# Optimization experiments

Hardware: AMD Instinct MI355X
Metric: run time of the kernel (lower is better)

## Reference

```python
import jax, jax.numpy as jnp
import numpy as np

N_NODES = 100000
N_EDGES = 3200000
N_GRAPHS = 512
DIM_H = 128
N_LAYERS = 3
N_CLASSES = 10
BN_EPS = 1e-5


def setup_inputs() -> dict:
    key = jax.random.key(0)
    ks = jax.random.split(key, 16)
    s = 1.0 / np.sqrt(DIM_H)
    x = jax.random.normal(ks[0], (N_NODES, DIM_H), dtype=jnp.float32)
    edge_index = jax.random.randint(ks[1], (2, N_EDGES), 0, N_NODES, dtype=jnp.int64)
    batch = jnp.sort(jax.random.randint(ks[2], (N_NODES,), 0, N_GRAPHS, dtype=jnp.int64))
    W1 = jax.random.uniform(ks[3], (N_LAYERS, DIM_H, DIM_H), jnp.float32, -s, s)
    b1 = jax.random.uniform(ks[4], (N_LAYERS, DIM_H), jnp.float32, -s, s)
    gamma = jnp.ones((N_LAYERS, DIM_H), jnp.float32)
    beta = jnp.zeros((N_LAYERS, DIM_H), jnp.float32)
    rmean = 0.1 * jax.random.normal(ks[5], (N_LAYERS, DIM_H), dtype=jnp.float32)
    rvar = jax.random.uniform(ks[6], (N_LAYERS, DIM_H), jnp.float32, 0.5, 1.5)
    W2 = jax.random.uniform(ks[7], (N_LAYERS, DIM_H, DIM_H), jnp.float32, -s, s)
    b2 = jax.random.uniform(ks[8], (N_LAYERS, DIM_H), jnp.float32, -s, s)
    dcat = DIM_H * N_LAYERS
    sf = 1.0 / np.sqrt(dcat)
    Wfin = jax.random.uniform(ks[9], (dcat, dcat), jnp.float32, -sf, sf)
    bfin = jax.random.uniform(ks[10], (dcat,), jnp.float32, -sf, sf)
    Wout = jax.random.uniform(ks[11], (dcat, N_CLASSES), jnp.float32, -sf, sf)
    bout = jax.random.uniform(ks[12], (N_CLASSES,), jnp.float32, -sf, sf)
    return {"x": x, "edge_index": edge_index, "batch": batch, "num_layers": N_LAYERS,
            "W1": W1, "b1": b1, "gamma": gamma, "beta": beta, "rmean": rmean, "rvar": rvar,
            "W2": W2, "b2": b2, "Wfin": Wfin, "bfin": bfin, "Wout": Wout, "bout": bout}


def reference(x, edge_index, batch, num_layers, W1, b1, gamma, beta, rmean, rvar, W2, b2, Wfin, bfin, Wout, bout):
    src, dst = edge_index[0], edge_index[1]
    h = x
    pooled = []
    for i in range(num_layers):
        # GINConv (eps=0): MLP(x + sum_{j in N(i)} x_j)
        aggr = jax.ops.segment_sum(h[src], dst, num_segments=N_NODES)
        z = (h + aggr) @ W1[i] + b1[i]
        # BatchNorm1d in eval mode (running stats)
        z = gamma[i] * (z - rmean[i]) * jax.lax.rsqrt(rvar[i] + BN_EPS) + beta[i]
        z = jax.nn.relu(z)
        h = jax.nn.relu(z @ W2[i] + b2[i])
        # global_add_pool: segment-sum over graph ids
        pooled.append(jax.ops.segment_sum(h, batch, num_segments=N_GRAPHS))
    h_fin = jnp.concatenate(pooled, axis=1)  # [G, dim_h*num_layers]
    h_fin = jax.nn.relu(h_fin @ Wfin + bfin)
    # dropout p=0.5 is identity in eval mode
    logits = h_fin @ Wout + bout
    return logits, jax.nn.log_softmax(logits, axis=1)
```

## Files before the change

### kernel.cpp

```cpp
#include <hip/hip_runtime.h>
#include <stdint.h>

#define N_NODES 100000
#define N_EDGES 3200000
#define N_GRAPHS 512
#define DIM 128
#define M_PAD 100096
#define NGB (M_PAD / 256)
#define NBUCK 391
#define CAP 9216
#define TILE 4096
#define NTILE 782
#define XMM_NB 392

typedef __bf16 bf16x8 __attribute__((ext_vector_type(8)));
typedef float f32x4 __attribute__((ext_vector_type(4)));

__device__ __forceinline__ unsigned short f2bf(float f) {
  unsigned u = __float_as_uint(f);
  u = u + 0x7FFFu + ((u >> 16) & 1u);
  return (unsigned short)(u >> 16);
}
__device__ __forceinline__ float bflo(unsigned v) { return __uint_as_float(v << 16); }
__device__ __forceinline__ float bfhi(unsigned v) { return __uint_as_float(v & 0xFFFF0000u); }
__device__ __forceinline__ float bfs(unsigned short v) { return __uint_as_float(((unsigned)v) << 16); }
__device__ __forceinline__ unsigned packbf(float a, float b) {
  return (unsigned)f2bf(a) | ((unsigned)f2bf(b) << 16);
}

__global__ void k_zero32(int* __restrict__ p, int n) {
  int i = blockIdx.x * 256 + threadIdx.x;
  if (i < n) p[i] = 0;
}

__global__ __launch_bounds__(256) void k_bucket(const int* __restrict__ ei,
                                                int* __restrict__ cnt,
                                                unsigned* __restrict__ rec) {
  __shared__ int hist[NBUCK];
  __shared__ int curs[NBUCK];
  int t = threadIdx.x;
  int base_e = blockIdx.x * TILE;
  int es[16], ed[16];
#pragma unroll
  for (int k = 0; k < 16; ++k) {
    int e = base_e + k * 256 + t;
    if (e < N_EDGES) { es[k] = ei[e]; ed[k] = ei[N_EDGES + e]; }
    else ed[k] = -1;
  }
  for (int i = t; i < NBUCK; i += 256) hist[i] = 0;
  __syncthreads();
#pragma unroll
  for (int k = 0; k < 16; ++k)
    if (ed[k] >= 0) atomicAdd(&hist[ed[k] >> 8], 1);
  __syncthreads();
  for (int i = t; i < NBUCK; i += 256) {
    int h = hist[i];
    int g = h ? atomicAdd(&cnt[i], h) : 0;
    curs[i] = i * CAP + g;
  }
  __syncthreads();
#pragma unroll
  for (int k = 0; k < 16; ++k) {
    if (ed[k] >= 0) {
      int b = ed[k] >> 8;
      int pos = atomicAdd(&curs[b], 1);
      rec[pos] = ((unsigned)es[k] << 8) | (unsigned)(ed[k] & 255);
    }
  }
}

__global__ __launch_bounds__(512) void k_bscan(const int* __restrict__ cnt,
                                               int* __restrict__ bbase,
                                               int* __restrict__ row_ptr) {
  __shared__ int sc[512];
  int t = threadIdx.x;
  int tot = (t < NBUCK) ? min(cnt[t], CAP) : 0;
  sc[t] = tot; __syncthreads();
  for (int off = 1; off < 512; off <<= 1) {
    int x = (t >= off) ? sc[t - off] : 0;
    __syncthreads();
    sc[t] += x;
    __syncthreads();
  }
  if (t < NBUCK) bbase[t] = sc[t] - tot;
  if (t == NBUCK - 1) {
    bbase[NBUCK] = sc[t];
    row_ptr[N_NODES] = sc[t];
  }
}

__global__ __launch_bounds__(256) void k_build(const unsigned* __restrict__ rec,
                                               const int* __restrict__ cnt,
                                               const int* __restrict__ bbase,
                                               int* __restrict__ row_ptr,
                                               int* __restrict__ col) {
  __shared__ int hist[256];
  __shared__ int sc[256];
  __shared__ int curs[256];
  int b = blockIdx.x, t = threadIdx.x;
  int n = min(cnt[b], CAP);
  const unsigned* p = rec + (size_t)b * CAP;
  hist[t] = 0; __syncthreads();
  for (int i = t; i < n; i += 256) atomicAdd(&hist[p[i] & 255u], 1);
  __syncthreads();
  int v = hist[t];
  sc[t] = v; __syncthreads();
  for (int off = 1; off < 256; off <<= 1) {
    int x = (t >= off) ? sc[t - off] : 0;
    __syncthreads();
    sc[t] += x;
    __syncthreads();
  }
  int excl = bbase[b] + sc[t] - v;
  int node = (b << 8) + t;
  if (node < N_NODES) row_ptr[node] = excl;
  curs[t] = excl;
  __syncthreads();
  for (int i = t; i < n; i += 256) {
    unsigned w = p[i];
    int pos = atomicAdd(&curs[w & 255u], 1);
    col[pos] = (int)(w >> 8);
  }
}

__global__ __launch_bounds__(256) void k_xmm1(const float* __restrict__ x,
                                              float* __restrict__ pmax,
                                              float* __restrict__ pmin) {
  __shared__ float smx[8][32][4];
  __shared__ float smn[8][32][4];
  int t = threadIdx.x;
  int c4 = t & 31;
  int ro = t >> 5;
  float mx0 = 0.f, mx1 = 0.f, mx2 = 0.f, mx3 = 0.f;
  float mn0 = 0.f, mn1 = 0.f, mn2 = 0.f, mn3 = 0.f;
  for (int row = blockIdx.x * 8 + ro; row < N_NODES; row += XMM_NB * 8) {
    float4 v = ((const float4*)x)[(size_t)row * 32 + c4];
    mx0 = fmaxf(mx0, v.x); mn0 = fmaxf(mn0, -v.x);
    mx1 = fmaxf(mx1, v.y); mn1 = fmaxf(mn1, -v.y);
    mx2 = fmaxf(mx2, v.z); mn2 = fmaxf(mn2, -v.z);
    mx3 = fmaxf(mx3, v.w); mn3 = fmaxf(mn3, -v.w);
  }
  smx[ro][c4][0] = mx0; smx[ro][c4][1] = mx1; smx[ro][c4][2] = mx2; smx[ro][c4][3] = mx3;
  smn[ro][c4][0] = mn0; smn[ro][c4][1] = mn1; smn[ro][c4][2] = mn2; smn[ro][c4][3] = mn3;
  __syncthreads();
  for (int off = 4; off > 0; off >>= 1) {
    if (ro < off) {
#pragma unroll
      for (int k = 0; k < 4; ++k) {
        smx[ro][c4][k] = fmaxf(smx[ro][c4][k], smx[ro + off][c4][k]);
        smn[ro][c4][k] = fmaxf(smn[ro][c4][k], smn[ro + off][c4][k]);
      }
    }
    __syncthreads();
  }
  if (ro == 0) {
#pragma unroll
    for (int k = 0; k < 4; ++k) {
      pmax[blockIdx.x * 128 + c4 * 4 + k] = smx[0][c4][k];
      pmin[blockIdx.x * 128 + c4 * 4 + k] = smn[0][c4][k];
    }
  }
}

__global__ __launch_bounds__(64) void k_xmm2(const float* __restrict__ pmax,
                                             const float* __restrict__ pmin,
                                             float* __restrict__ xmx,
                                             float* __restrict__ xminf) {
  int c = blockIdx.x & 127;
  int isMin = blockIdx.x >> 7;
  const float* src = isMin ? pmin : pmax;
  int l = threadIdx.x;
  float m = 0.f;
  for (int p2 = l; p2 < XMM_NB; p2 += 64) m = fmaxf(m, src[p2 * 128 + c]);
#pragma unroll
  for (int off = 32; off > 0; off >>= 1) m = fmaxf(m, __shfl_down(m, off));
  if (l == 0) {
    if (isMin) xminf[c] = -m;
    else xmx[c] = m;
  }
}

__global__ __launch_bounds__(64) void k_hred(const float* __restrict__ pmaxb,
                                             float* __restrict__ hmax) {
  int c = blockIdx.x;
  float m = 0.f;
  for (int b = threadIdx.x; b < NGB; b += 64) m = fmaxf(m, pmaxb[(size_t)b * 128 + c]);
#pragma unroll
  for (int off = 32; off > 0; off >>= 1) m = fmaxf(m, __shfl_down(m, off));
  if (threadIdx.x == 0) hmax[c] = m;
}

__global__ void k_convx(const float* __restrict__ x, const float* __restrict__ qmin,
                        const float* __restrict__ qmax, unsigned short* __restrict__ xq) {
  int i = blockIdx.x * 256 + threadIdx.x;
  if (i >= M_PAD * 64) return;
  int lane = i & 63;
  unsigned short o = 0;
  if ((i >> 6) < N_NODES) {
    float mn0 = qmin[2 * lane], mn1 = qmin[2 * lane + 1];
    float r0 = qmax[2 * lane] - mn0, r1 = qmax[2 * lane + 1] - mn1;
    float is0 = r0 > 1e-20f ? 255.f / r0 : 0.f;
    float is1 = r1 > 1e-20f ? 255.f / r1 : 0.f;
    float2 f = ((const float2*)x)[i];
    int q0 = (int)rintf((f.x - mn0) * is0); q0 = min(max(q0, 0), 255);
    int q1 = (int)rintf((f.y - mn1) * is1); q1 = min(max(q1, 0), 255);
    o = (unsigned short)(q0 | (q1 << 8));
  }
  xq[i] = o;
}

__global__ void k_quant(const unsigned* __restrict__ hbf, const float* __restrict__ qmax,
                        unsigned short* __restrict__ hq) {
  int i = blockIdx.x * 256 + threadIdx.x;
  if (i >= M_PAD * 64) return;
  int lane = i & 63;
  float mx0 = qmax[2 * lane], mx1 = qmax[2 * lane + 1];
  float is0 = mx0 > 1e-20f ? 255.f / mx0 : 0.f;
  float is1 = mx1 > 1e-20f ? 255.f / mx1 : 0.f;
  unsigned v = hbf[i];
  int q0 = (int)rintf(bflo(v) * is0); q0 = min(max(q0, 0), 255);
  int q1 = (int)rintf(bfhi(v) * is1); q1 = min(max(q1, 0), 255);
  hq[i] = (unsigned short)(q0 | (q1 << 8));
}

__global__ void k_convw(const float* __restrict__ W1, const float* __restrict__ W2,
                        unsigned short* __restrict__ Wt1, unsigned short* __restrict__ Wt2) {
  int i = blockIdx.x * 256 + threadIdx.x;
  if (i >= 3 * DIM * DIM) return;
  int l = i >> 14, rem = i & 16383, k = rem >> 7, n = rem & 127;
  int o = (l << 14) + (n << 7) + k;
  Wt1[o] = f2bf(W1[i]);
  Wt2[o] = f2bf(W2[i]);
}

__global__ void k_coef(const float* __restrict__ b1, const float* __restrict__ gamma,
                       const float* __restrict__ beta, const float* __restrict__ rmean,
                       const float* __restrict__ rvar, const float* __restrict__ b2,
                       float* __restrict__ sA1, float* __restrict__ sB1,
                       float* __restrict__ sA2, float* __restrict__ sB2) {
  int i = blockIdx.x * 128 + threadIdx.x;
  if (i >= 3 * DIM) return;
  float sa = gamma[i] * rsqrtf(rvar[i] + 1e-5f);
  sA1[i] = sa;
  sB1[i] = fmaf(sa, b1[i] - rmean[i], beta[i]);
  sA2[i] = 1.0f;
  sB2[i] = b2[i];
}

__global__ __launch_bounds__(256) void k_aggr(const unsigned short* __restrict__ hq,
                                              const int* __restrict__ row_ptr,
                                              const int* __restrict__ col,
                                              const float* __restrict__ qmin,
                                              const float* __restrict__ qmax,
                                              unsigned* __restrict__ tmp) {
  const unsigned* hq32 = (const unsigned*)hq;
  int wv = (blockIdx.x << 2) + (threadIdx.x >> 6);
  int lane = threadIdx.x & 63;
  int dw = lane & 31;
  bool hi = lane >= 32;
  if (wv >= M_PAD) return;
  if (wv >= N_NODES) {
    ((uint2*)(tmp + (size_t)wv * 64))[dw] = make_uint2(0u, 0u);
    return;
  }
  unsigned ae = 0u, ao = 0u;
  int s = __builtin_amdgcn_readfirstlane(row_ptr[wv]);
  int e = __builtin_amdgcn_readfirstlane(row_ptr[wv + 1]);
  for (int base = s; base < e; base += 64) {
    int n = e - base; if (n > 64) n = 64;
    int cv = (lane < n) ? col[base + lane] : 0;
    int np = n >> 1;
    int j = 0;
    for (; j + 8 <= np; j += 8) {
#pragma unroll
      for (int u = 0; u < 8; ++u) {
        int s0 = __builtin_amdgcn_readlane(cv, 2 * (j + u));
        int s1 = __builtin_amdgcn_readlane(cv, 2 * (j + u) + 1);
        unsigned v = hq32[(hi ? s1 : s0) * 32 + dw];
        ae += v & 0x00FF00FFu;
        ao += (v >> 8) & 0x00FF00FFu;
      }
    }
    for (; j < np; ++j) {
      int s0 = __builtin_amdgcn_readlane(cv, 2 * j);
      int s1 = __builtin_amdgcn_readlane(cv, 2 * j + 1);
      unsigned v = hq32[(hi ? s1 : s0) * 32 + dw];
      ae += v & 0x00FF00FFu;
      ao += (v >> 8) & 0x00FF00FFu;
    }
    if (n & 1) {
      int c = __builtin_amdgcn_readlane(cv, n - 1);
      unsigned v = hq32[c * 32 + dw];
      if (hi) v = 0u;
      ae += v & 0x00FF00FFu;
      ao += (v >> 8) & 0x00FF00FFu;
    }
  }
  ae += __shfl_xor(ae, 32);
  ao += __shfl_xor(ao, 32);
  {
    unsigned v = hq32[wv * 32 + dw];
    ae += v & 0x00FF00FFu;
    ao += (v >> 8) & 0x00FF00FFu;
  }
  if (lane < 32) {
    float cnt = (float)(e - s + 1);
    float4 qn = ((const float4*)qmin)[dw];
    float4 qx = ((const float4*)qmax)[dw];
    const float k255 = 1.0f / 255.0f;
    float A0 = fmaf(qn.x, cnt, (qx.x - qn.x) * k255 * (float)(ae & 0xFFFFu));
    float A1 = fmaf(qn.y, cnt, (qx.y - qn.y) * k255 * (float)(ao & 0xFFFFu));
    float A2 = fmaf(qn.z, cnt, (qx.z - qn.z) * k255 * (float)(ae >> 16));
    float A3 = fmaf(qn.w, cnt, (qx.w - qn.w) * k255 * (float)(ao >> 16));
    ((uint2*)(tmp + (size_t)wv * 64))[dw] = make_uint2(packbf(A0, A1), packbf(A2, A3));
  }
}

__global__ __launch_bounds__(256, 2) void k_gemm12(const unsigned short* __restrict__ A,
                                                   const unsigned short* __restrict__ Wt1,
                                                   const float* __restrict__ sA1,
                                                   const float* __restrict__ sB1,
                                                   const unsigned short* __restrict__ Wt2,
                                                   const float* __restrict__ sA2,
                                                   const float* __restrict__ sB2,
                                                   const int* __restrict__ batch,
                                                   unsigned short* __restrict__ out,
                                                   float* __restrict__ pooled8, int layer,
                                                   float* __restrict__ pmaxb, int do_max) {
  __shared__ unsigned short zt[4][64][136];
  __shared__ float colred[128];
  __shared__ int sgid[256];
  int w = threadIdx.x >> 6, lane = threadIdx.x & 63;
  int q = lane >> 4, n16 = lane & 15;
  int rbase = (blockIdx.x << 8) + (w << 6);
  if (do_max && threadIdx.x < 128) colred[threadIdx.x] = 0.f;
  {
    int rr = (blockIdx.x << 8) + threadIdx.x;
    sgid[threadIdx.x] = (rr < N_NODES) ? batch[rr] : -1;
  }

  {
    bf16x8 Bf[4][8];
#pragma unroll
    for (int ks = 0; ks < 4; ++ks)
#pragma unroll
      for (int c = 0; c < 8; ++c)
        Bf[ks][c] = *(const bf16x8*)(Wt1 + (size_t)((c << 4) + n16) * DIM + ks * 32 + q * 8);
#pragma unroll
    for (int t = 0; t < 4; ++t) {
      int r0 = rbase + (t << 4);
      f32x4 acc[8] = {};
#pragma unroll
      for (int ks = 0; ks < 4; ++ks) {
        bf16x8 a = *(const bf16x8*)(A + (size_t)(r0 + n16) * DIM + ks * 32 + q * 8);
#pragma unroll
        for (int c = 0; c < 8; ++c)
          acc[c] = __builtin_amdgcn_mfma_f32_16x16x32_bf16(a, Bf[ks][c], acc[c], 0, 0, 0);
      }
#pragma unroll
      for (int c = 0; c < 8; ++c) {
        int colc = (c << 4) + n16;
        float s = sA1[colc], tt = sB1[colc];
#pragma unroll
        for (int r = 0; r < 4; ++r) {
          float v = fmaxf(fmaf(s, acc[c][r], tt), 0.0f);
          zt[w][(t << 4) + (q << 2) + r][colc] = f2bf(v);
        }
      }
    }
  }

  float mcol[8];
#pragma unroll
  for (int c = 0; c < 8; ++c) mcol[c] = 0.f;
  {
    bf16x8 Bf[4][8];
#pragma unroll
    for (int ks = 0; ks < 4; ++ks)
#pragma unroll
      for (int c = 0; c < 8; ++c)
        Bf[ks][c] = *(const bf16x8*)(Wt2 + (size_t)((c << 4) + n16) * DIM + ks * 32 + q * 8);
#pragma unroll
    for (int t = 0; t < 4; ++t) {
      int r0 = rbase + (t << 4);
      f32x4 acc[8] = {};
#pragma unroll
      for (int ks = 0; ks < 4; ++ks) {
        bf16x8 a = *(const bf16x8*)(&zt[w][(t << 4) + n16][ks * 32 + q * 8]);
#pragma unroll
        for (int c = 0; c < 8; ++c)
          acc[c] = __builtin_amdgcn_mfma_f32_16x16x32_bf16(a, Bf[ks][c], acc[c], 0, 0, 0);
      }
      __builtin_amdgcn_s_waitcnt(0);
#pragma unroll
      for (int c = 0; c < 8; ++c) {
        int colc = (c << 4) + n16;
        float s = sA2[colc], tt = sB2[colc];
#pragma unroll
        for (int r = 0; r < 4; ++r) {
          float v = fmaxf(fmaf(s, acc[c][r], tt), 0.0f);
          mcol[c] = fmaxf(mcol[c], v);
          unsigned short hv = f2bf(v);
          out[(size_t)(r0 + (q << 2) + r) * DIM + colc] = hv;
          zt[w][(t << 4) + (q << 2) + r][colc] = hv;
        }
      }
    }
  }
  __syncthreads();

  {
    const unsigned short* ztf = &zt[0][0][0];
    int colp = threadIdx.x & 127, grp = threadIdx.x >> 7;
    int cp = blockIdx.x & 7;
    float pacc = 0.f;
    int gcur = sgid[grp << 7];
    for (int r = 0; r < 128; ++r) {
      int row = (grp << 7) + r;
      int g = sgid[row];
      if (g != gcur) {
        if (gcur >= 0)
          atomicAdd(&pooled8[((size_t)cp * N_GRAPHS + gcur) * 384 + layer * DIM + colp], pacc);
        pacc = 0.f; gcur = g;
      }
      if (g >= 0) pacc += bfs(ztf[row * 136 + colp]);
    }
    if (gcur >= 0)
      atomicAdd(&pooled8[((size_t)cp * N_GRAPHS + gcur) * 384 + layer * DIM + colp], pacc);
  }

  if (do_max) {
#pragma unroll
    for (int c = 0; c < 8; ++c)
      atomicMax((int*)&colred[(c << 4) + n16], __float_as_int(mcol[c]));
    __syncthreads();
    if (threadIdx.x < 128)
      pmaxb[(size_t)blockIdx.x * 128 + threadIdx.x] = colred[threadIdx.x];
  }
}

__global__ __launch_bounds__(384) void k_head(const float* __restrict__ pooled8,
                                              const float* __restrict__ Wfin,
                                              const float* __restrict__ bfin,
                                              const float* __restrict__ Wout,
                                              const float* __restrict__ bout,
                                              float* __restrict__ out) {
  __shared__ float p[8][384];
  __shared__ float hf[8][392];
  __shared__ float lg[8][10];
  __shared__ float lse[8];
  int t = threadIdx.x, g0 = blockIdx.x << 3;
  for (int i = t; i < 8 * 384; i += 384) {
    int gl = i / 384, k = i % 384;
    float s = 0.f;
#pragma unroll
    for (int cp = 0; cp < 8; ++cp)
      s += pooled8[((size_t)cp * N_GRAPHS + g0 + gl) * 384 + k];
    p[gl][k] = s;
  }
  __syncthreads();
  float bb = bfin[t];
  float acc[8];
#pragma unroll
  for (int g = 0; g < 8; ++g) acc[g] = bb;
  for (int k = 0; k < 384; ++k) {
    float wv = Wfin[k * 384 + t];
#pragma unroll
    for (int g = 0; g < 8; ++g) acc[g] = fmaf(p[g][k], wv, acc[g]);
  }
#pragma unroll
  for (int g = 0; g < 8; ++g) hf[g][t] = fmaxf(acc[g], 0.f);
  __syncthreads();
  if (t < 80) {
    int g = t / 10, c = t % 10;
    float a = bout[c];
    for (int k = 0; k < 384; ++k) a = fmaf(hf[g][k], Wout[k * 10 + c], a);
    lg[g][c] = a;
  }
  __syncthreads();
  if (t < 8) {
    float m = lg[t][0];
#pragma unroll
    for (int i = 1; i < 10; ++i) m = fmaxf(m, lg[t][i]);
    float ss = 0.f;
#pragma unroll
    for (int i = 0; i < 10; ++i) ss += __expf(lg[t][i] - m);
    lse[t] = m + __logf(ss);
  }
  __syncthreads();
  if (t < 80) {
    int g = t / 10, c = t % 10;
    out[(size_t)(g0 + g) * 10 + c] = lg[g][c];
    out[(size_t)N_GRAPHS * 10 + (size_t)(g0 + g) * 10 + c] = lg[g][c] - lse[g];
  }
}

extern "C" void kernel_launch(void* const* d_in, const int* in_sizes, int n_in,
                              void* d_out, int out_size, void* d_ws, size_t ws_size,
                              hipStream_t stream) {
  const float* x     = (const float*)d_in[0];
  const int*   ei    = (const int*)d_in[1];
  const int*   batch = (const int*)d_in[2];
  const float* W1    = (const float*)d_in[4];
  const float* b1    = (const float*)d_in[5];
  const float* gamma = (const float*)d_in[6];
  const float* beta  = (const float*)d_in[7];
  const float* rmean = (const float*)d_in[8];
  const float* rvar  = (const float*)d_in[9];
  const float* W2    = (const float*)d_in[10];
  const float* b2    = (const float*)d_in[11];
  const float* Wfin  = (const float*)d_in[12];
  const float* bfin  = (const float*)d_in[13];
  const float* Wout  = (const float*)d_in[14];
  const float* bout  = (const float*)d_in[15];
  float* out = (float*)d_out;

  char* p = (char*)d_ws;
  auto alloc = [&](size_t bytes) { char* r = p; p += (bytes + 255) & ~255ull; return r; };
  int* cnt      = (int*)alloc(NBUCK * 4);
  unsigned* rec = (unsigned*)alloc((size_t)NBUCK * CAP * 4);
  int* bbase    = (int*)alloc((NBUCK + 1) * 4);
  int* row_ptr  = (int*)alloc((N_NODES + 1) * 4);
  int* colb     = (int*)alloc((size_t)N_EDGES * 4);
  unsigned short* xq  = (unsigned short*)alloc((size_t)M_PAD * 64 * 2);
  unsigned short* hqb = (unsigned short*)alloc((size_t)M_PAD * 64 * 2);
  unsigned* hbf  = (unsigned*)alloc((size_t)M_PAD * 64 * 4);
  unsigned* tmpb = (unsigned*)alloc((size_t)M_PAD * 64 * 4);
  unsigned short* Wt1 = (unsigned short*)alloc(3 * DIM * DIM * 2);
  unsigned short* Wt2 = (unsigned short*)alloc(3 * DIM * DIM * 2);
  float* pmax   = (float*)alloc((size_t)XMM_NB * 128 * 4);
  float* pmin   = (float*)alloc((size_t)XMM_NB * 128 * 4);
  float* pmaxb  = (float*)alloc((size_t)NGB * 128 * 4);
  float* sA1    = (float*)alloc(384 * 4);
  float* sB1    = (float*)alloc(384 * 4);
  float* sA2    = (float*)alloc(384 * 4);
  float* sB2    = (float*)alloc(384 * 4);
  float* qbuf   = (float*)alloc(1024 * 4);
  float* xmx    = qbuf + 128;
  float* xminf  = qbuf + 256;
  float* hmax0  = qbuf + 384;
  float* hmax1  = qbuf + 512;
  float* zeros  = qbuf + 640;
  float* pooled8 = (float*)alloc((size_t)8 * N_GRAPHS * 384 * 4);

  k_zero32<<<(NBUCK + 255) / 256, 256, 0, stream>>>(cnt, NBUCK);
  k_zero32<<<4, 256, 0, stream>>>((int*)qbuf, 1024);
  k_zero32<<<(8 * N_GRAPHS * 384 + 255) / 256, 256, 0, stream>>>((int*)pooled8, 8 * N_GRAPHS * 384);

  k_bucket<<<NTILE, 256, 0, stream>>>(ei, cnt, rec);
  k_bscan<<<1, 512, 0, stream>>>(cnt, bbase, row_ptr);
  k_build<<<NBUCK, 256, 0, stream>>>(rec, cnt, bbase, row_ptr, colb);

  k_xmm1<<<XMM_NB, 256, 0, stream>>>(x, pmax, pmin);
  k_xmm2<<<256, 64, 0, stream>>>(pmax, pmin, xmx, xminf);
  k_convx<<<(M_PAD * 64 + 255) / 256, 256, 0, stream>>>(x, xminf, xmx, xq);
  k_convw<<<(3 * DIM * DIM + 255) / 256, 256, 0, stream>>>(W1, W2, Wt1, Wt2);
  k_coef<<<3, 128, 0, stream>>>(b1, gamma, beta, rmean, rvar, b2, sA1, sB1, sA2, sB2);

  k_aggr<<<M_PAD / 4, 256, 0, stream>>>(xq, row_ptr, colb, xminf, xmx, tmpb);
  k_gemm12<<<NGB, 256, 0, stream>>>((const unsigned short*)tmpb, Wt1, sA1, sB1,
                                    Wt2, sA2, sB2, batch, (unsigned short*)hbf,
                                    pooled8, 0, pmaxb, 1);
  k_hred<<<128, 64, 0, stream>>>(pmaxb, hmax0);
  k_quant<<<(M_PAD * 64 + 255) / 256, 256, 0, stream>>>(hbf, hmax0, hqb);
  k_aggr<<<M_PAD / 4, 256, 0, stream>>>(hqb, row_ptr, colb, zeros, hmax0, tmpb);
  k_gemm12<<<NGB, 256, 0, stream>>>((const unsigned short*)tmpb, Wt1 + DIM * DIM,
                                    sA1 + DIM, sB1 + DIM, Wt2 + DIM * DIM,
                                    sA2 + DIM, sB2 + DIM, batch, (unsigned short*)hbf,
                                    pooled8, 1, pmaxb, 1);
  k_hred<<<128, 64, 0, stream>>>(pmaxb, hmax1);
  k_quant<<<(M_PAD * 64 + 255) / 256, 256, 0, stream>>>(hbf, hmax1, hqb);
  k_aggr<<<M_PAD / 4, 256, 0, stream>>>(hqb, row_ptr, colb, zeros, hmax1, tmpb);
  k_gemm12<<<NGB, 256, 0, stream>>>((const unsigned short*)tmpb, Wt1 + 2 * DIM * DIM,
                                    sA1 + 2 * DIM, sB1 + 2 * DIM, Wt2 + 2 * DIM * DIM,
                                    sA2 + 2 * DIM, sB2 + 2 * DIM, batch, (unsigned short*)hbf,
                                    pooled8, 2, pmaxb, 0);

  k_head<<<N_GRAPHS / 8, 384, 0, stream>>>(pooled8, Wfin, bfin, Wout, bout, out);
}
```

Baseline: 659.3 us.

## Gather neighbor rows with 128-bit loads, eight edges per wave step

Rewrites the per-node neighbor aggregation so each wave handles 32 edges per iteration. Lanes split into 8 groups of 8, and each lane loads 16-byte chunks of the quantized rows, replacing the readlane-serialized 4-byte gathers. Out-of-range edges are pointed at a zeroed padding row, which k_quant now clears explicitly. This adds a cross-lane shuffle reduction and a bpermute redistribution at the end in exchange for fewer, wider memory requests.

```diff
diff --git a/kernel.cpp b/kernel.cpp
--- a/kernel.cpp
+++ b/kernel.cpp
@@ -213,6 +213,7 @@
                         unsigned short* __restrict__ hq) {
   int i = blockIdx.x * 256 + threadIdx.x;
   if (i >= M_PAD * 64) return;
+  if ((i >> 6) >= N_NODES) { hq[i] = 0; return; }
   int lane = i & 63;
   float mx0 = qmax[2 * lane], mx1 = qmax[2 * lane + 1];
   float is0 = mx0 > 1e-20f ? 255.f / mx0 : 0.f;
@@ -253,66 +254,93 @@
                                               const float* __restrict__ qmin,
                                               const float* __restrict__ qmax,
                                               unsigned* __restrict__ tmp) {
+  const uint4* hq128 = (const uint4*)hq;
   const unsigned* hq32 = (const unsigned*)hq;
   int wv = (blockIdx.x << 2) + (threadIdx.x >> 6);
   int lane = threadIdx.x & 63;
+  int grp = lane >> 3;
+  int lo8 = lane & 7;
   int dw = lane & 31;
-  bool hi = lane >= 32;
   if (wv >= M_PAD) return;
   if (wv >= N_NODES) {
     ((uint2*)(tmp + (size_t)wv * 64))[dw] = make_uint2(0u, 0u);
     return;
   }
-  unsigned ae = 0u, ao = 0u;
+  unsigned ae0 = 0, ae1 = 0, ae2 = 0, ae3 = 0;
+  unsigned ao0 = 0, ao1 = 0, ao2 = 0, ao3 = 0;
   int s = __builtin_amdgcn_readfirstlane(row_ptr[wv]);
   int e = __builtin_amdgcn_readfirstlane(row_ptr[wv + 1]);
-  for (int base = s; base < e; base += 64) {
-    int n = e - base; if (n > 64) n = 64;
-    int cv = (lane < n) ? col[base + lane] : 0;
-    int np = n >> 1;
-    int j = 0;
-    for (; j + 8 <= np; j += 8) {
-#pragma unroll
-      for (int u = 0; u < 8; ++u) {
-        int s0 = __builtin_amdgcn_readlane(cv, 2 * (j + u));
-        int s1 = __builtin_amdgcn_readlane(cv, 2 * (j + u) + 1);
-        unsigned v = hq32[(hi ? s1 : s0) * 32 + dw];
-        ae += v & 0x00FF00FFu;
-        ao += (v >> 8) & 0x00FF00FFu;
-      }
-    }
-    for (; j < np; ++j) {
-      int s0 = __builtin_amdgcn_readlane(cv, 2 * j);
-      int s1 = __builtin_amdgcn_readlane(cv, 2 * j + 1);
-      unsigned v = hq32[(hi ? s1 : s0) * 32 + dw];
+  int pidx = (lo8 << 3) + grp;
+  for (int base = s; base < e; base += 32) {
+    int n = e - base; if (n > 32) n = 32;
+    int cv = (pidx < n) ? col[base + pidx] : 0;
+    int s0 = __builtin_amdgcn_ds_swizzle(cv, 0x18);
+    int s1 = __builtin_amdgcn_ds_swizzle(cv, 0x38);
+    int s2 = __builtin_amdgcn_ds_swizzle(cv, 0x58);
+    int s3 = __builtin_amdgcn_ds_swizzle(cv, 0x78);
+    s0 = (grp      < n) ? s0 : N_NODES;
+    s1 = (grp +  8 < n) ? s1 : N_NODES;
+    s2 = (grp + 16 < n) ? s2 : N_NODES;
+    s3 = (grp + 24 < n) ? s3 : N_NODES;
+    uint4 v0 = hq128[s0 * 8 + lo8];
+    uint4 v1 = hq128[s1 * 8 + lo8];
+    uint4 v2 = hq128[s2 * 8 + lo8];
+    uint4 v3 = hq128[s3 * 8 + lo8];
+    ae0 += v0.x & 0x00FF00FFu; ao0 += (v0.x >> 8) & 0x00FF00FFu;
+    ae1 += v0.y & 0x00FF00FFu; ao1 += (v0.y >> 8) & 0x00FF00FFu;
+    ae2 += v0.z & 0x00FF00FFu; ao2 += (v0.z >> 8) & 0x00FF00FFu;
+    ae3 += v0.w & 0x00FF00FFu; ao3 += (v0.w >> 8) & 0x00FF00FFu;
+    ae0 += v1.x & 0x00FF00FFu; ao0 += (v1.x >> 8) & 0x00FF00FFu;
+    ae1 += v1.y & 0x00FF00FFu; ao1 += (v1.y >> 8) & 0x00FF00FFu;
+    ae2 += v1.z & 0x00FF00FFu; ao2 += (v1.z >> 8) & 0x00FF00FFu;
+    ae3 += v1.w & 0x00FF00FFu; ao3 += (v1.w >> 8) & 0x00FF00FFu;
+    ae0 += v2.x & 0x00FF00FFu; ao0 += (v2.x >> 8) & 0x00FF00FFu;
+    ae1 += v2.y & 0x00FF00FFu; ao1 += (v2.y >> 8) & 0x00FF00FFu;
+    ae2 += v2.z & 0x00FF00FFu; ao2 += (v2.z >> 8) & 0x00FF00FFu;
+    ae3 += v2.w & 0x00FF00FFu; ao3 += (v2.w >> 8) & 0x00FF00FFu;
+    ae0 += v3.x & 0x00FF00FFu; ao0 += (v3.x >> 8) & 0x00FF00FFu;
+    ae1 += v3.y & 0x00FF00FFu; ao1 += (v3.y >> 8) & 0x00FF00FFu;
+    ae2 += v3.z & 0x00FF00FFu; ao2 += (v3.z >> 8) & 0x00FF00FFu;
+    ae3 += v3.w & 0x00FF00FFu; ao3 += (v3.w >> 8) & 0x00FF00FFu;
+  }
+  ae0 += __shfl_xor(ae0, 8); ae0 += __shfl_xor(ae0, 16); ae0 += __shfl_xor(ae0, 32);
+  ae1 += __shfl_xor(ae1, 8); ae1 += __shfl_xor(ae1, 16); ae1 += __shfl_xor(ae1, 32);
+  ae2 += __shfl_xor(ae2, 8); ae2 += __shfl_xor(ae2, 16); ae2 += __shfl_xor(ae2, 32);
+  ae3 += __shfl_xor(ae3, 8); ae3 += __shfl_xor(ae3, 16); ae3 += __shfl_xor(ae3, 32);
+  ao0 += __shfl_xor(ao0, 8); ao0 += __shfl_xor(ao0, 16); ao0 += __shfl_xor(ao0, 32);
+  ao1 += __shfl_xor(ao1, 8); ao1 += __shfl_xor(ao1, 16); ao1 += __shfl_xor(ao1, 32);
+  ao2 += __shfl_xor(ao2, 8); ao2 += __shfl_xor(ao2, 16); ao2 += __shfl_xor(ao2, 32);
+  ao3 += __shfl_xor(ao3, 8); ao3 += __shfl_xor(ao3, 16); ao3 += __shfl_xor(ao3, 32);
+  {
+    int ba = ((dw >> 2) & 7) << 2;
+    unsigned f0 = (unsigned)__builtin_amdgcn_ds_bpermute(ba, (int)ae0);
+    unsigned f1 = (unsigned)__builtin_amdgcn_ds_bpermute(ba, (int)ae1);
+    unsigned f2 = (unsigned)__builtin_amdgcn_ds_bpermute(ba, (int)ae2);
+    unsigned f3 = (unsigned)__builtin_amdgcn_ds_bpermute(ba, (int)ae3);
+    unsigned g0 = (unsigned)__builtin_amdgcn_ds_bpermute(ba, (int)ao0);
+    unsigned g1 = (unsigned)__builtin_amdgcn_ds_bpermute(ba, (int)ao1);
+    unsigned g2 = (unsigned)__builtin_amdgcn_ds_bpermute(ba, (int)ao2);
+    unsigned g3 = (unsigned)__builtin_amdgcn_ds_bpermute(ba, (int)ao3);
+    unsigned el = (dw & 1) ? f1 : f0;
+    unsigned eh = (dw & 1) ? f3 : f2;
+    unsigned ae = (dw & 2) ? eh : el;
+    unsigned ol = (dw & 1) ? g1 : g0;
+    unsigned oh = (dw & 1) ? g3 : g2;
+    unsigned ao = (dw & 2) ? oh : ol;
+    if (lane < 32) {
+      unsigned v = hq32[wv * 32 + dw];
       ae += v & 0x00FF00FFu;
       ao += (v >> 8) & 0x00FF00FFu;
+      float cntf = (float)(e - s + 1);
+      float4 qn = ((const float4*)qmin)[dw];
+      float4 qx = ((const float4*)qmax)[dw];
+      const float k255 = 1.0f / 255.0f;
+      float A0 = fmaf(qn.x, cntf, (qx.x - qn.x) * k255 * (float)(ae & 0xFFFFu));
+      float A1 = fmaf(qn.y, cntf, (qx.y - qn.y) * k255 * (float)(ao & 0xFFFFu));
+      float A2 = fmaf(qn.z, cntf, (qx.z - qn.z) * k255 * (float)(ae >> 16));
+      float A3 = fmaf(qn.w, cntf, (qx.w - qn.w) * k255 * (float)(ao >> 16));
+      ((uint2*)(tmp + (size_t)wv * 64))[dw] = make_uint2(packbf(A0, A1), packbf(A2, A3));
     }
-    if (n & 1) {
-      int c = __builtin_amdgcn_readlane(cv, n - 1);
-      unsigned v = hq32[c * 32 + dw];
-      if (hi) v = 0u;
-      ae += v & 0x00FF00FFu;
-      ao += (v >> 8) & 0x00FF00FFu;
-    }
-  }
-  ae += __shfl_xor(ae, 32);
-  ao += __shfl_xor(ao, 32);
-  {
-    unsigned v = hq32[wv * 32 + dw];
-    ae += v & 0x00FF00FFu;
-    ao += (v >> 8) & 0x00FF00FFu;
-  }
-  if (lane < 32) {
-    float cnt = (float)(e - s + 1);
-    float4 qn = ((const float4*)qmin)[dw];
-    float4 qx = ((const float4*)qmax)[dw];
-    const float k255 = 1.0f / 255.0f;
-    float A0 = fmaf(qn.x, cnt, (qx.x - qn.x) * k255 * (float)(ae & 0xFFFFu));
-    float A1 = fmaf(qn.y, cnt, (qx.y - qn.y) * k255 * (float)(ao & 0xFFFFu));
-    float A2 = fmaf(qn.z, cnt, (qx.z - qn.z) * k255 * (float)(ae >> 16));
-    float A3 = fmaf(qn.w, cnt, (qx.w - qn.w) * k255 * (float)(ao >> 16));
-    ((uint2*)(tmp + (size_t)wv * 64))[dw] = make_uint2(packbf(A0, A1), packbf(A2, A3));
   }
 }
 
```

After: 621.1 us. 5.8% less time.

## Split quantized features into column teams and aggregate one node per thread

Applied to the files above, without the earlier changes.

The quantized feature matrix is stored as four column slices, each 32 bytes per node, so that each thread can gather a whole node's slice with two 16-byte loads. The aggregation kernel changes from one wavefront per node to one thread per node per team. Each thread loops up to the wavefront's maximum degree, uses a zero padding row for edges past its own degree, and keeps packed 8-bit accumulators in registers. This aims to remove the per-edge readlane and shuffle overhead and issue wider gathers, at the cost of divergence from varying degrees, uncoalesced column-index loads and higher register pressure.

```diff
diff --git a/kernel.cpp b/kernel.cpp
--- a/kernel.cpp
+++ b/kernel.cpp
@@ -12,6 +12,8 @@
 #define TILE 4096
 #define NTILE 782
 #define XMM_NB 392
+#define NTEAM 4
+#define ZROW N_NODES
 
 typedef __bf16 bf16x8 __attribute__((ext_vector_type(8)));
 typedef float f32x4 __attribute__((ext_vector_type(4)));
@@ -195,8 +197,9 @@
   int i = blockIdx.x * 256 + threadIdx.x;
   if (i >= M_PAD * 64) return;
   int lane = i & 63;
+  int node = i >> 6;
   unsigned short o = 0;
-  if ((i >> 6) < N_NODES) {
+  if (node < N_NODES) {
     float mn0 = qmin[2 * lane], mn1 = qmin[2 * lane + 1];
     float r0 = qmax[2 * lane] - mn0, r1 = qmax[2 * lane + 1] - mn1;
     float is0 = r0 > 1e-20f ? 255.f / r0 : 0.f;
@@ -206,7 +209,7 @@
     int q1 = (int)rintf((f.y - mn1) * is1); q1 = min(max(q1, 0), 255);
     o = (unsigned short)(q0 | (q1 << 8));
   }
-  xq[i] = o;
+  xq[(size_t)(lane >> 4) * (M_PAD * 16) + (size_t)node * 16 + (lane & 15)] = o;
 }
 
 __global__ void k_quant(const unsigned* __restrict__ hbf, const float* __restrict__ qmax,
@@ -214,13 +217,16 @@
   int i = blockIdx.x * 256 + threadIdx.x;
   if (i >= M_PAD * 64) return;
   int lane = i & 63;
+  int node = i >> 6;
+  size_t oidx = (size_t)(lane >> 4) * (M_PAD * 16) + (size_t)node * 16 + (lane & 15);
+  if (node >= N_NODES) { hq[oidx] = 0; return; }
   float mx0 = qmax[2 * lane], mx1 = qmax[2 * lane + 1];
   float is0 = mx0 > 1e-20f ? 255.f / mx0 : 0.f;
   float is1 = mx1 > 1e-20f ? 255.f / mx1 : 0.f;
   unsigned v = hbf[i];
   int q0 = (int)rintf(bflo(v) * is0); q0 = min(max(q0, 0), 255);
   int q1 = (int)rintf(bfhi(v) * is1); q1 = min(max(q1, 0), 255);
-  hq[i] = (unsigned short)(q0 | (q1 << 8));
+  hq[oidx] = (unsigned short)(q0 | (q1 << 8));
 }
 
 __global__ void k_convw(const float* __restrict__ W1, const float* __restrict__ W2,
@@ -247,72 +253,80 @@
   sB2[i] = b2[i];
 }
 
+#define ACCP(v, E, O) { E += (v) & 0x00FF00FFu; O += ((v) >> 8) & 0x00FF00FFu; }
+
+__device__ __forceinline__ uint2 dq2(unsigned ev, unsigned od, float4 qn, float4 qx, float cntf) {
+  const float k255 = 1.0f / 255.0f;
+  float A0 = fmaf(qn.x, cntf, (qx.x - qn.x) * k255 * (float)(ev & 0xFFFFu));
+  float A1 = fmaf(qn.y, cntf, (qx.y - qn.y) * k255 * (float)(od & 0xFFFFu));
+  float A2 = fmaf(qn.z, cntf, (qx.z - qn.z) * k255 * (float)(ev >> 16));
+  float A3 = fmaf(qn.w, cntf, (qx.w - qn.w) * k255 * (float)(od >> 16));
+  return make_uint2(packbf(A0, A1), packbf(A2, A3));
+}
+
 __global__ __launch_bounds__(256) void k_aggr(const unsigned short* __restrict__ hq,
                                               const int* __restrict__ row_ptr,
                                               const int* __restrict__ col,
                                               const float* __restrict__ qmin,
                                               const float* __restrict__ qmax,
                                               unsigned* __restrict__ tmp) {
-  const unsigned* hq32 = (const unsigned*)hq;
-  int wv = (blockIdx.x << 2) + (threadIdx.x >> 6);
-  int lane = threadIdx.x & 63;
-  int dw = lane & 31;
-  bool hi = lane >= 32;
-  if (wv >= M_PAD) return;
-  if (wv >= N_NODES) {
-    ((uint2*)(tmp + (size_t)wv * 64))[dw] = make_uint2(0u, 0u);
-    return;
-  }
-  unsigned ae = 0u, ao = 0u;
-  int s = __builtin_amdgcn_readfirstlane(row_ptr[wv]);
-  int e = __builtin_amdgcn_readfirstlane(row_ptr[wv + 1]);
-  for (int base = s; base < e; base += 64) {
-    int n = e - base; if (n > 64) n = 64;
-    int cv = (lane < n) ? col[base + lane] : 0;
-    int np = n >> 1;
-    int j = 0;
-    for (; j + 8 <= np; j += 8) {
-#pragma unroll
-      for (int u = 0; u < 8; ++u) {
-        int s0 = __builtin_amdgcn_readlane(cv, 2 * (j + u));
-        int s1 = __builtin_amdgcn_readlane(cv, 2 * (j + u) + 1);
-        unsigned v = hq32[(hi ? s1 : s0) * 32 + dw];
-        ae += v & 0x00FF00FFu;
-        ao += (v >> 8) & 0x00FF00FFu;
-      }
-    }
-    for (; j < np; ++j) {
-      int s0 = __builtin_amdgcn_readlane(cv, 2 * j);
-      int s1 = __builtin_amdgcn_readlane(cv, 2 * j + 1);
-      unsigned v = hq32[(hi ? s1 : s0) * 32 + dw];
-      ae += v & 0x00FF00FFu;
-      ao += (v >> 8) & 0x00FF00FFu;
-    }
-    if (n & 1) {
-      int c = __builtin_amdgcn_readlane(cv, n - 1);
-      unsigned v = hq32[c * 32 + dw];
-      if (hi) v = 0u;
-      ae += v & 0x00FF00FFu;
-      ao += (v >> 8) & 0x00FF00FFu;
-    }
-  }
-  ae += __shfl_xor(ae, 32);
-  ao += __shfl_xor(ao, 32);
-  {
-    unsigned v = hq32[wv * 32 + dw];
-    ae += v & 0x00FF00FFu;
-    ao += (v >> 8) & 0x00FF00FFu;
-  }
-  if (lane < 32) {
-    float cnt = (float)(e - s + 1);
-    float4 qn = ((const float4*)qmin)[dw];
-    float4 qx = ((const float4*)qmax)[dw];
-    const float k255 = 1.0f / 255.0f;
-    float A0 = fmaf(qn.x, cnt, (qx.x - qn.x) * k255 * (float)(ae & 0xFFFFu));
-    float A1 = fmaf(qn.y, cnt, (qx.y - qn.y) * k255 * (float)(ao & 0xFFFFu));
-    float A2 = fmaf(qn.z, cnt, (qx.z - qn.z) * k255 * (float)(ae >> 16));
-    float A3 = fmaf(qn.w, cnt, (qx.w - qn.w) * k255 * (float)(ao >> 16));
-    ((uint2*)(tmp + (size_t)wv * 64))[dw] = make_uint2(packbf(A0, A1), packbf(A2, A3));
+  int team = blockIdx.x & (NTEAM - 1);
+  int nr = blockIdx.x >> 2;
+  int node = (nr << 8) + threadIdx.x;
+  const uint4* hs = (const uint4*)((const unsigned short*)hq + (size_t)team * (M_PAD * 16));
+  bool valid = node < N_NODES;
+  int s = valid ? row_ptr[node] : 0;
+  int e = valid ? row_ptr[node + 1] : 0;
+  int deg = e - s;
+  int dmax = deg;
+#pragma unroll
+  for (int off = 32; off > 0; off >>= 1) dmax = max(dmax, __shfl_xor(dmax, off));
+
+  unsigned ev[8], od[8];
+#pragma unroll
+  for (int g = 0; g < 8; ++g) { ev[g] = 0u; od[g] = 0u; }
+
+  for (int e0 = 0; e0 < dmax; e0 += 4) {
+    int c[4];
+#pragma unroll
+    for (int u = 0; u < 4; ++u)
+      c[u] = (e0 + u < deg) ? col[s + e0 + u] : ZROW;
+    uint4 ga[4], gb[4];
+#pragma unroll
+    for (int u = 0; u < 4; ++u) {
+      ga[u] = hs[(size_t)c[u] * 2];
+      gb[u] = hs[(size_t)c[u] * 2 + 1];
+    }
+#pragma unroll
+    for (int u = 0; u < 4; ++u) {
+      ACCP(ga[u].x, ev[0], od[0]); ACCP(ga[u].y, ev[1], od[1]);
+      ACCP(ga[u].z, ev[2], od[2]); ACCP(ga[u].w, ev[3], od[3]);
+      ACCP(gb[u].x, ev[4], od[4]); ACCP(gb[u].y, ev[5], od[5]);
+      ACCP(gb[u].z, ev[6], od[6]); ACCP(gb[u].w, ev[7], od[7]);
+    }
+  }
+
+  uint4* dst = (uint4*)(tmp + (size_t)node * 64 + team * 16);
+  if (valid) {
+    uint4 sa = hs[(size_t)node * 2];
+    uint4 sb = hs[(size_t)node * 2 + 1];
+    ACCP(sa.x, ev[0], od[0]); ACCP(sa.y, ev[1], od[1]);
+    ACCP(sa.z, ev[2], od[2]); ACCP(sa.w, ev[3], od[3]);
+    ACCP(sb.x, ev[4], od[4]); ACCP(sb.y, ev[5], od[5]);
+    ACCP(sb.z, ev[6], od[6]); ACCP(sb.w, ev[7], od[7]);
+    float cntf = (float)(deg + 1);
+    const float4* qnp = (const float4*)qmin + team * 8;
+    const float4* qxp = (const float4*)qmax + team * 8;
+    uint2 r[8];
+#pragma unroll
+    for (int g = 0; g < 8; ++g) r[g] = dq2(ev[g], od[g], qnp[g], qxp[g], cntf);
+    dst[0] = make_uint4(r[0].x, r[0].y, r[1].x, r[1].y);
+    dst[1] = make_uint4(r[2].x, r[2].y, r[3].x, r[3].y);
+    dst[2] = make_uint4(r[4].x, r[4].y, r[5].x, r[5].y);
+    dst[3] = make_uint4(r[6].x, r[6].y, r[7].x, r[7].y);
+  } else {
+    uint4 z = make_uint4(0u, 0u, 0u, 0u);
+    dst[0] = z; dst[1] = z; dst[2] = z; dst[3] = z;
   }
 }
 
@@ -521,7 +535,7 @@
   unsigned* rec = (unsigned*)alloc((size_t)NBUCK * CAP * 4);
   int* bbase    = (int*)alloc((NBUCK + 1) * 4);
   int* row_ptr  = (int*)alloc((N_NODES + 1) * 4);
-  int* colb     = (int*)alloc((size_t)N_EDGES * 4);
+  int* colb     = (int*)alloc(((size_t)N_EDGES + 256) * 4);
   unsigned short* xq  = (unsigned short*)alloc((size_t)M_PAD * 64 * 2);
   unsigned short* hqb = (unsigned short*)alloc((size_t)M_PAD * 64 * 2);
   unsigned* hbf  = (unsigned*)alloc((size_t)M_PAD * 64 * 4);
@@ -557,20 +571,20 @@
   k_convw<<<(3 * DIM * DIM + 255) / 256, 256, 0, stream>>>(W1, W2, Wt1, Wt2);
   k_coef<<<3, 128, 0, stream>>>(b1, gamma, beta, rmean, rvar, b2, sA1, sB1, sA2, sB2);
 
-  k_aggr<<<M_PAD / 4, 256, 0, stream>>>(xq, row_ptr, colb, xminf, xmx, tmpb);
+  k_aggr<<<NGB * NTEAM, 256, 0, stream>>>(xq, row_ptr, colb, xminf, xmx, tmpb);
   k_gemm12<<<NGB, 256, 0, stream>>>((const unsigned short*)tmpb, Wt1, sA1, sB1,
                                     Wt2, sA2, sB2, batch, (unsigned short*)hbf,
                                     pooled8, 0, pmaxb, 1);
   k_hred<<<128, 64, 0, stream>>>(pmaxb, hmax0);
   k_quant<<<(M_PAD * 64 + 255) / 256, 256, 0, stream>>>(hbf, hmax0, hqb);
-  k_aggr<<<M_PAD / 4, 256, 0, stream>>>(hqb, row_ptr, colb, zeros, hmax0, tmpb);
+  k_aggr<<<NGB * NTEAM, 256, 0, stream>>>(hqb, row_ptr, colb, zeros, hmax0, tmpb);
   k_gemm12<<<NGB, 256, 0, stream>>>((const unsigned short*)tmpb, Wt1 + DIM * DIM,
                                     sA1 + DIM, sB1 + DIM, Wt2 + DIM * DIM,
                                     sA2 + DIM, sB2 + DIM, batch, (unsigned short*)hbf,
                                     pooled8, 1, pmaxb, 1);
   k_hred<<<128, 64, 0, stream>>>(pmaxb, hmax1);
   k_quant<<<(M_PAD * 64 + 255) / 256, 256, 0, stream>>>(hbf, hmax1, hqb);
-  k_aggr<<<M_PAD / 4, 256, 0, stream>>>(hqb, row_ptr, colb, zeros, hmax1, tmpb);
+  k_aggr<<<NGB * NTEAM, 256, 0, stream>>>(hqb, row_ptr, colb, zeros, hmax1, tmpb);
   k_gemm12<<<NGB, 256, 0, stream>>>((const unsigned short*)tmpb, Wt1 + 2 * DIM * DIM,
                                     sA1 + 2 * DIM, sB1 + 2 * DIM, Wt2 + 2 * DIM * DIM,
                                     sA2 + 2 * DIM, sB2 + 2 * DIM, batch, (unsigned short*)hbf,
```

New measurement: 1.130 ms. +71.4%, slower.
